# Optimization experiments

Hardware: AMD Instinct MI355X
Metric: run time of the kernel (lower is better)

## Reference

```python
import jax, jax.numpy as jnp
import numpy as np


def setup_inputs() -> dict:
    key = jax.random.key(0)
    k1, k2 = jax.random.split(key)
    support_features = jax.random.normal(k1, (1000, 5, 512), dtype=jnp.float32)
    query_features = jax.random.normal(k2, (5000, 512), dtype=jnp.float32)
    return {"support_features": support_features, "query_features": query_features, "use_cosine": 1}


def reference(support_features, query_features, use_cosine):
    # Preprocess: mean-center over (classes, shots), then L2-normalize per vector.
    mean = jnp.mean(support_features, axis=(0, 1), keepdims=True)  # [1,1,D]
    s = support_features - mean                                    # [C,S,D]
    q = query_features - mean[0]                                   # [Q,D]
    s = s / jnp.linalg.norm(s, axis=2, keepdims=True)
    q = q / jnp.linalg.norm(q, axis=1, keepdims=True)
    if use_cosine:
        # cosine sims without materializing [C,Q,S,D]; einsum fuses the dot.
        sims = jnp.einsum('csd,qd->cqs', s, q)   # [C,Q,S]
        best = jnp.max(sims, axis=2)             # [C,Q] best shot per class
        return jnp.argmax(best, axis=0)          # [Q] predicted class
    else:
        # euclidean cdist(query[Q,D], support[C,S,D]) -> [C,Q,S]
        d2 = (jnp.sum(q * q, axis=1)[None, :, None]
              + jnp.sum(s * s, axis=2)[:, None, :]
              - 2.0 * jnp.einsum('csd,qd->cqs', s, q))
        dist = jnp.sqrt(jnp.maximum(d2, 0.0))
        best = jnp.min(dist, axis=2)
        return jnp.argmin(best, axis=0)
```

## Files before the change

kernel.cpp:

```cpp
#include <hip/hip_runtime.h>
#include <stdint.h>

#define D     512
#define NSUP  5000
#define NQRY  5000
#define NPAD  5120
#define MEAN_BLOCKS 100
#define ROWS_PER_MEAN_BLOCK 50
#define SCALE 512.0f

#define OFF_SHI     0
#define OFF_SLO     5242880
#define OFF_QHI     10485760
#define OFF_QLO     15728640
#define OFF_PARTIAL 20971520
#define OFF_MEAN    21176320
#define OFF_KEYS    21178368

#define SH_SHI   0
#define SH_SLO   32768
#define SH_QHI   65536
#define SH_QLO   98304
#define SH_KL    131072
#define SH_TOTAL (131072 + 2048)

typedef _Float16 half4v __attribute__((ext_vector_type(4)));
typedef _Float16 half8v __attribute__((ext_vector_type(8)));
typedef float    f32x4  __attribute__((ext_vector_type(4)));

__device__ __forceinline__ unsigned long long pack_key(float v, int sidx) {
    unsigned u = __float_as_uint(v);
    u = (u & 0x80000000u) ? ~u : (u | 0x80000000u);
    return ((unsigned long long)u << 32) | (unsigned)(0xFFFFFFFFu - (unsigned)sidx);
}

__device__ __forceinline__ void gload16(const void* g, void* l) {
    __builtin_amdgcn_global_load_lds(
        (const __attribute__((address_space(1))) unsigned int*)g,
        (__attribute__((address_space(3))) unsigned int*)l, 16, 0, 0);
}

__global__ void k_partial_mean(const float* __restrict__ sup, float* __restrict__ partial) {
    const int col = threadIdx.x;
    const int b   = blockIdx.x;
    const int r0  = b * ROWS_PER_MEAN_BLOCK;
    float acc = 0.0f;
    #pragma unroll 5
    for (int r = 0; r < ROWS_PER_MEAN_BLOCK; ++r)
        acc += sup[(size_t)(r0 + r) * D + col];
    partial[b * D + col] = acc;
}

__global__ void k_mean_init(const float* __restrict__ partial, float* __restrict__ mean,
                            unsigned long long* __restrict__ keys) {
    const int col = threadIdx.x;
    float acc = 0.0f;
    #pragma unroll 4
    for (int b = 0; b < MEAN_BLOCKS; ++b) acc += partial[b * D + col];
    mean[col] = acc * (1.0f / (float)NSUP);
    for (int i = col; i < NSUP; i += 512) keys[i] = 0ull;
}

__global__ void k_split(const float* __restrict__ sup, const float* __restrict__ qry,
                        const float* __restrict__ mean,
                        _Float16* __restrict__ shi, _Float16* __restrict__ slo,
                        _Float16* __restrict__ qhi, _Float16* __restrict__ qlo) {
    const int t    = threadIdx.x;
    const int rloc = t >> 7;
    const int tc   = t & 127;
    const int b    = (int)blockIdx.x * 4 + rloc;
    const float* src; _Float16 *dhi, *dlo; int valid;
    if (b < NPAD) { src = sup + (size_t)b * D;
                    dhi = shi + (size_t)b * D; dlo = slo + (size_t)b * D; valid = (b < NSUP); }
    else          { int r = b - NPAD; src = qry + (size_t)r * D;
                    dhi = qhi + (size_t)r * D; dlo = qlo + (size_t)r * D; valid = (r < NQRY); }
    __shared__ float red[8];
    if (!valid) {
        half4v z = {};
        *(half4v*)(dhi + tc * 4) = z;
        *(half4v*)(dlo + tc * 4) = z;
        return;
    }
    float4 v = *(const float4*)(src + tc * 4);
    float4 m = *(const float4*)(mean + tc * 4);
    v.x -= m.x; v.y -= m.y; v.z -= m.z; v.w -= m.w;
    float ss = v.x * v.x + v.y * v.y + v.z * v.z + v.w * v.w;
    #pragma unroll
    for (int off = 32; off > 0; off >>= 1) ss += __shfl_down(ss, off, 64);
    if ((t & 63) == 0) red[t >> 6] = ss;
    __syncthreads();
    const float rn = SCALE / sqrtf(red[rloc * 2] + red[rloc * 2 + 1]);
    float sv[4] = {v.x * rn, v.y * rn, v.z * rn, v.w * rn};
    half4v h, l;
    #pragma unroll
    for (int i = 0; i < 4; ++i) {
        _Float16 hh = (_Float16)sv[i];
        h[i] = hh;
        l[i] = (_Float16)(sv[i] - (float)hh);
    }
    *(half4v*)(dhi + tc * 4) = h;
    *(half4v*)(dlo + tc * 4) = l;
}

__launch_bounds__(512, 2)
__global__ void k_main(const _Float16* __restrict__ shi, const _Float16* __restrict__ slo,
                       const _Float16* __restrict__ qhi, const _Float16* __restrict__ qlo,
                       unsigned long long* __restrict__ keys) {
    extern __shared__ char smem[];
    char* lshi = smem + SH_SHI;
    char* lslo = smem + SH_SLO;
    char* lqhi = smem + SH_QHI;
    char* lqlo = smem + SH_QLO;
    unsigned long long* kl = (unsigned long long*)(smem + SH_KL);

    const int tid  = threadIdx.x;
    const int lane = tid & 63;
    const int wv   = tid >> 6;
    const int q0   = blockIdx.x * 256;
    const int s0   = blockIdx.y * 256;
    const int wr   = wv >> 2;
    const int wc   = wv & 3;

    if (tid < 256) kl[tid] = 0ull;

    const int srow = wv * 16 + (lane >> 2);
    const int sl0  = ((lane & 3) ^ ((lane >> 3) & 3)) * 16;
    const size_t gA0 = (size_t)(s0 + srow) * 1024 + sl0;
    const size_t gB0 = (size_t)(q0 + srow) * 1024 + sl0;
    const char* pShi = (const char*)shi; const char* pSlo = (const char*)slo;
    const char* pQhi = (const char*)qhi; const char* pQlo = (const char*)qlo;
    const int dst0 = wv * 1024;
    const int dst1 = 8192 + wv * 1024;

    const int l15 = lane & 15;
    const int kg  = lane >> 4;
    const int swz = (kg ^ ((l15 >> 1) & 3)) * 16;
    const int foA = (wr * 128 + l15) * 64 + swz;
    const int foB = (wc * 64  + l15) * 64 + swz;

    f32x4 acc[8][4] = {};

#define BAR()    asm volatile("s_barrier" ::: "memory")
#define WAITV0() asm volatile("s_waitcnt vmcnt(0)" ::: "memory")
#define WAITL()  asm volatile("s_waitcnt lgkmcnt(0)" ::: "memory")

#define STAGE_A(P, KT) do { const size_t kb_ = (size_t)(KT) * 64;           \
        gload16(pShi + gA0 + kb_,          lshi + (P) * 16384 + dst0);      \
        gload16(pShi + gA0 + 131072 + kb_, lshi + (P) * 16384 + dst1);      \
        gload16(pSlo + gA0 + kb_,          lslo + (P) * 16384 + dst0);      \
    } while (0)
#define STAGE_B(P, KT) do { const size_t kb_ = (size_t)(KT) * 64;           \
        gload16(pSlo + gA0 + 131072 + kb_, lslo + (P) * 16384 + dst1);      \
        gload16(pQhi + gB0 + kb_,          lqhi + (P) * 16384 + dst0);      \
        gload16(pQhi + gB0 + 131072 + kb_, lqhi + (P) * 16384 + dst1);      \
    } while (0)
#define STAGE_C(P, KT) do { const size_t kb_ = (size_t)(KT) * 64;           \
        gload16(pQlo + gB0 + kb_,          lqlo + (P) * 16384 + dst0);      \
        gload16(pQlo + gB0 + 131072 + kb_, lqlo + (P) * 16384 + dst1);      \
    } while (0)

#define RD_A(P, QA) do { _Pragma("unroll")                                  \
        for (int i_ = 0; i_ < 4; ++i_) {                                    \
            ah[i_] = *(const half8v*)(lshi + (P)*16384 + foA + ((QA)*4 + i_)*1024); \
            al[i_] = *(const half8v*)(lslo + (P)*16384 + foA + ((QA)*4 + i_)*1024); \
        } } while (0)

#define RD_B(P, QB, BH, BL) do { _Pragma("unroll")                          \
        for (int j_ = 0; j_ < 2; ++j_) {                                    \
            BH[j_] = *(const half8v*)(lqhi + (P)*16384 + foB + ((QB)*2 + j_)*1024); \
            BL[j_] = *(const half8v*)(lqlo + (P)*16384 + foB + ((QB)*2 + j_)*1024); \
        } } while (0)

#define MMA_Q(QA, QB, BH, BL) do {                                          \
        __builtin_amdgcn_s_setprio(1);                                      \
        _Pragma("unroll")                                                   \
        for (int i_ = 0; i_ < 4; ++i_)                                      \
        { _Pragma("unroll")                                                 \
          for (int j_ = 0; j_ < 2; ++j_) {                                  \
            f32x4* a_ = &acc[(QA)*4 + i_][(QB)*2 + j_];                     \
            *a_ = __builtin_amdgcn_mfma_f32_16x16x32_f16(ah[i_], BH[j_], *a_, 0, 0, 0); \
            *a_ = __builtin_amdgcn_mfma_f32_16x16x32_f16(ah[i_], BL[j_], *a_, 0, 0, 0); \
            *a_ = __builtin_amdgcn_mfma_f32_16x16x32_f16(al[i_], BH[j_], *a_, 0, 0, 0); \
          } }                                                               \
        __builtin_amdgcn_s_setprio(0);                                      \
        __builtin_amdgcn_sched_barrier(0);                                  \
    } while (0)

    STAGE_A(0, 0); STAGE_B(0, 0); STAGE_C(0, 0);
    WAITV0();
    BAR();

    for (int t = 0; t < 16; ++t) {
        const int P    = t & 1;
        const int Pn   = P ^ 1;
        const int n    = t + 1;
        const bool more = (n < 16);
        half8v ah[4], al[4], bh0[2], bl0[2], bh1[2], bl1[2];

        RD_A(P, 0);
        RD_B(P, 0, bh0, bl0);
        if (more) STAGE_A(Pn, n);
        BAR(); WAITL();
        MMA_Q(0, 0, bh0, bl0);
        BAR();

        RD_B(P, 1, bh1, bl1);
        if (more) STAGE_B(Pn, n);
        BAR(); WAITL();
        MMA_Q(0, 1, bh1, bl1);
        BAR();

        RD_A(P, 1);
        if (more) STAGE_C(Pn, n);
        BAR(); WAITL();
        MMA_Q(1, 0, bh0, bl0);
        BAR();

        MMA_Q(1, 1, bh1, bl1);
        WAITV0();
        BAR();
    }

#undef MMA_Q
#undef RD_B
#undef RD_A
#undef STAGE_C
#undef STAGE_B
#undef STAGE_A

    #pragma unroll
    for (int fb = 0; fb < 4; ++fb) {
        unsigned long long best = 0ull;
        #pragma unroll
        for (int fa = 0; fa < 8; ++fa)
            #pragma unroll
            for (int r = 0; r < 4; ++r) {
                const int s = s0 + wr * 128 + fa * 16 + kg * 4 + r;
                if (s < NSUP) {
                    unsigned long long k = pack_key(acc[fa][fb][r], s);
                    if (k > best) best = k;
                }
            }
        unsigned long long o = __shfl_xor(best, 16, 64); if (o > best) best = o;
        o = __shfl_xor(best, 32, 64);                    if (o > best) best = o;
        if (kg == 0) atomicMax(&kl[wc * 64 + fb * 16 + l15], best);
    }
    __syncthreads();
    if (tid < 256) {
        const int q = q0 + tid;
        if (q < NQRY && kl[tid] != 0ull) atomicMax(&keys[q], kl[tid]);
    }
}

__global__ void k_decode(const unsigned long long* __restrict__ keys, int* __restrict__ out) {
    const int q = blockIdx.x * 256 + threadIdx.x;
    if (q < NQRY) {
        unsigned sidx = 0xFFFFFFFFu - (unsigned)(keys[q] & 0xFFFFFFFFull);
        out[q] = (int)(sidx / 5u);
    }
}

extern "C" void kernel_launch(void* const* d_in, const int* in_sizes, int n_in,
                              void* d_out, int out_size, void* d_ws, size_t ws_size,
                              hipStream_t stream) {
    const float* sup = (const float*)d_in[0];
    const float* qry = (const float*)d_in[1];
    int* out = (int*)d_out;

    char* ws = (char*)d_ws;
    _Float16* shi = (_Float16*)(ws + OFF_SHI);
    _Float16* slo = (_Float16*)(ws + OFF_SLO);
    _Float16* qhi = (_Float16*)(ws + OFF_QHI);
    _Float16* qlo = (_Float16*)(ws + OFF_QLO);
    float* partial = (float*)(ws + OFF_PARTIAL);
    float* mean    = (float*)(ws + OFF_MEAN);
    unsigned long long* keys = (unsigned long long*)(ws + OFF_KEYS);

    static bool attr_set = false;
    if (!attr_set) {
        (void)hipFuncSetAttribute((const void*)k_main,
                                  hipFuncAttributeMaxDynamicSharedMemorySize, SH_TOTAL);
        attr_set = true;
    }

    k_partial_mean<<<MEAN_BLOCKS, 512, 0, stream>>>(sup, partial);
    k_mean_init<<<1, 512, 0, stream>>>(partial, mean, keys);
    k_split<<<(2 * NPAD) / 4, 512, 0, stream>>>(sup, qry, mean, shi, slo, qhi, qlo);
    dim3 grid(NPAD / 256, NPAD / 256);
    k_main<<<grid, 512, SH_TOTAL, stream>>>(shi, slo, qhi, qlo, keys);
    k_decode<<<(NQRY + 255) / 256, 256, 0, stream>>>(keys, out);
}
```

Measured before the change: 165.7 us.

## Split main loop into eight finer MFMA phases with interleaved staging

Restructures the double-buffered K loop from four coarse phases (each 24 MFMAs) into eight phases of 12 MFMAs. Global-to-LDS staging is now issued in four equal chunks spread across the first four phases, and A fragments are read from LDS two rows at a time. The last iteration reloads tile 0 instead of branching, which removes the `more` condition at the cost of redundant loads. The aim is finer interleaving of LDS reads, global loads and MFMA work to hide latency. The price is twice as many barriers per iteration, including some back-to-back barriers with no work between them.

```diff
diff --git a/kernel.cpp b/kernel.cpp
--- a/kernel.cpp
+++ b/kernel.cpp
@@ -144,26 +144,27 @@
 #define WAITV0() asm volatile("s_waitcnt vmcnt(0)" ::: "memory")
 #define WAITL()  asm volatile("s_waitcnt lgkmcnt(0)" ::: "memory")
 
-#define STAGE_A(P, KT) do { const size_t kb_ = (size_t)(KT) * 64;           \
-        gload16(pShi + gA0 + kb_,          lshi + (P) * 16384 + dst0);      \
-        gload16(pShi + gA0 + 131072 + kb_, lshi + (P) * 16384 + dst1);      \
-        gload16(pSlo + gA0 + kb_,          lslo + (P) * 16384 + dst0);      \
+#define ST2(P, KT, K2) do { const size_t kb_ = (size_t)(KT) * 64;           \
+        if ((K2) == 0) {                                                    \
+            gload16(pShi + gA0 + kb_,          lshi + (P) * 16384 + dst0);  \
+            gload16(pShi + gA0 + 131072 + kb_, lshi + (P) * 16384 + dst1);  \
+        } else if ((K2) == 1) {                                             \
+            gload16(pSlo + gA0 + kb_,          lslo + (P) * 16384 + dst0);  \
+            gload16(pSlo + gA0 + 131072 + kb_, lslo + (P) * 16384 + dst1);  \
+        } else if ((K2) == 2) {                                             \
+            gload16(pQhi + gB0 + kb_,          lqhi + (P) * 16384 + dst0);  \
+            gload16(pQhi + gB0 + 131072 + kb_, lqhi + (P) * 16384 + dst1);  \
+        } else {                                                            \
+            gload16(pQlo + gB0 + kb_,          lqlo + (P) * 16384 + dst0);  \
+            gload16(pQlo + gB0 + 131072 + kb_, lqlo + (P) * 16384 + dst1);  \
+        } } while (0)
+
+#define RD_A2(P, FA, AI) do {                                               \
+        ah[AI]   = *(const half8v*)(lshi + (P)*16384 + foA + (FA)*1024);    \
+        al[AI]   = *(const half8v*)(lslo + (P)*16384 + foA + (FA)*1024);    \
+        ah[AI+1] = *(const half8v*)(lshi + (P)*16384 + foA + (FA+1)*1024);  \
+        al[AI+1] = *(const half8v*)(lslo + (P)*16384 + foA + (FA+1)*1024);  \
     } while (0)
-#define STAGE_B(P, KT) do { const size_t kb_ = (size_t)(KT) * 64;           \
-        gload16(pSlo + gA0 + 131072 + kb_, lslo + (P) * 16384 + dst1);      \
-        gload16(pQhi + gB0 + kb_,          lqhi + (P) * 16384 + dst0);      \
-        gload16(pQhi + gB0 + 131072 + kb_, lqhi + (P) * 16384 + dst1);      \
-    } while (0)
-#define STAGE_C(P, KT) do { const size_t kb_ = (size_t)(KT) * 64;           \
-        gload16(pQlo + gB0 + kb_,          lqlo + (P) * 16384 + dst0);      \
-        gload16(pQlo + gB0 + 131072 + kb_, lqlo + (P) * 16384 + dst1);      \
-    } while (0)
-
-#define RD_A(P, QA) do { _Pragma("unroll")                                  \
-        for (int i_ = 0; i_ < 4; ++i_) {                                    \
-            ah[i_] = *(const half8v*)(lshi + (P)*16384 + foA + ((QA)*4 + i_)*1024); \
-            al[i_] = *(const half8v*)(lslo + (P)*16384 + foA + ((QA)*4 + i_)*1024); \
-        } } while (0)
 
 #define RD_B(P, QB, BH, BL) do { _Pragma("unroll")                          \
         for (int j_ = 0; j_ < 2; ++j_) {                                    \
@@ -171,62 +172,53 @@
             BL[j_] = *(const half8v*)(lqlo + (P)*16384 + foB + ((QB)*2 + j_)*1024); \
         } } while (0)
 
-#define MMA_Q(QA, QB, BH, BL) do {                                          \
+#define MMA12(R0, AI, C0, BH, BL) do {                                      \
         __builtin_amdgcn_s_setprio(1);                                      \
         _Pragma("unroll")                                                   \
-        for (int i_ = 0; i_ < 4; ++i_)                                      \
+        for (int i_ = 0; i_ < 2; ++i_)                                      \
         { _Pragma("unroll")                                                 \
           for (int j_ = 0; j_ < 2; ++j_) {                                  \
-            f32x4* a_ = &acc[(QA)*4 + i_][(QB)*2 + j_];                     \
-            *a_ = __builtin_amdgcn_mfma_f32_16x16x32_f16(ah[i_], BH[j_], *a_, 0, 0, 0); \
-            *a_ = __builtin_amdgcn_mfma_f32_16x16x32_f16(ah[i_], BL[j_], *a_, 0, 0, 0); \
-            *a_ = __builtin_amdgcn_mfma_f32_16x16x32_f16(al[i_], BH[j_], *a_, 0, 0, 0); \
+            f32x4* a_ = &acc[(R0) + i_][(C0) + j_];                         \
+            *a_ = __builtin_amdgcn_mfma_f32_16x16x32_f16(ah[(AI)+i_], BH[j_], *a_, 0, 0, 0); \
+            *a_ = __builtin_amdgcn_mfma_f32_16x16x32_f16(ah[(AI)+i_], BL[j_], *a_, 0, 0, 0); \
+            *a_ = __builtin_amdgcn_mfma_f32_16x16x32_f16(al[(AI)+i_], BH[j_], *a_, 0, 0, 0); \
           } }                                                               \
         __builtin_amdgcn_s_setprio(0);                                      \
         __builtin_amdgcn_sched_barrier(0);                                  \
     } while (0)
 
-    STAGE_A(0, 0); STAGE_B(0, 0); STAGE_C(0, 0);
+    ST2(0, 0, 0); ST2(0, 0, 1); ST2(0, 0, 2); ST2(0, 0, 3);
     WAITV0();
     BAR();
 
     for (int t = 0; t < 16; ++t) {
-        const int P    = t & 1;
-        const int Pn   = P ^ 1;
-        const int n    = t + 1;
-        const bool more = (n < 16);
+        const int P  = t & 1;
+        const int Pn = P ^ 1;
+        const int tn = (t + 1 < 16) ? (t + 1) : 0;
         half8v ah[4], al[4], bh0[2], bl0[2], bh1[2], bl1[2];
 
-        RD_A(P, 0);
-        RD_B(P, 0, bh0, bl0);
-        if (more) STAGE_A(Pn, n);
-        BAR(); WAITL();
-        MMA_Q(0, 0, bh0, bl0);
-        BAR();
-
-        RD_B(P, 1, bh1, bl1);
-        if (more) STAGE_B(Pn, n);
-        BAR(); WAITL();
-        MMA_Q(0, 1, bh1, bl1);
-        BAR();
-
-        RD_A(P, 1);
-        if (more) STAGE_C(Pn, n);
-        BAR(); WAITL();
-        MMA_Q(1, 0, bh0, bl0);
-        BAR();
-
-        MMA_Q(1, 1, bh1, bl1);
+        RD_A2(P, 0, 0); RD_B(P, 0, bh0, bl0); ST2(Pn, tn, 0);
+        BAR(); WAITL(); MMA12(0, 0, 0, bh0, bl0); BAR();
+        RD_A2(P, 2, 2); ST2(Pn, tn, 1);
+        BAR(); WAITL(); MMA12(2, 2, 0, bh0, bl0); BAR();
+        RD_B(P, 1, bh1, bl1); ST2(Pn, tn, 2);
+        BAR(); WAITL(); MMA12(0, 0, 2, bh1, bl1); BAR();
+        ST2(Pn, tn, 3);
+        BAR(); MMA12(2, 2, 2, bh1, bl1); BAR();
+        RD_A2(P, 4, 0);
+        BAR(); WAITL(); MMA12(4, 0, 0, bh0, bl0); BAR();
+        RD_A2(P, 6, 2);
+        BAR(); WAITL(); MMA12(6, 2, 0, bh0, bl0); BAR();
+        BAR(); MMA12(4, 0, 2, bh1, bl1); BAR();
+        BAR(); MMA12(6, 2, 2, bh1, bl1);
         WAITV0();
         BAR();
     }
 
-#undef MMA_Q
+#undef MMA12
 #undef RD_B
-#undef RD_A
-#undef STAGE_C
-#undef STAGE_B
-#undef STAGE_A
+#undef RD_A2
+#undef ST2
 
     #pragma unroll
     for (int fb = 0; fb < 4; ++fb) {
```

New measurement: 165.4 us. About the same (-0.1%).
